# Optimization experiments

Hardware: AMD Instinct MI355X
Metric: run time of the kernel (lower is better)

## Reference

```python
import math
import jax, jax.numpy as jnp
import numpy as np

B, CIN, H, W = 1, 64, 56, 56
MID, HEADS, COUT, MPOS = 32, 8, 64, 56


def setup_inputs() -> dict:
    key = jax.random.key(0)
    ks = jax.random.split(key, 11)
    s = 0.05
    return {
        "x": jax.random.normal(ks[0], (B, CIN, H, W), jnp.float32),
        "Wq": jax.random.normal(ks[1], (MID * HEADS, CIN), jnp.float32) * s,
        "bq": jax.random.normal(ks[2], (MID * HEADS,), jnp.float32) * s,
        "Wk": jax.random.normal(ks[3], (MID * HEADS, CIN), jnp.float32) * s,
        "bk": jax.random.normal(ks[4], (MID * HEADS,), jnp.float32) * s,
        "Wv": jax.random.normal(ks[5], (MID * HEADS, CIN), jnp.float32) * s,
        "bv": jax.random.normal(ks[6], (MID * HEADS,), jnp.float32) * s,
        "Wo": jax.random.normal(ks[7], (COUT, MID * HEADS), jnp.float32) * s,
        "bo": jax.random.normal(ks[8], (COUT,), jnp.float32) * s,
        "row_emb_table": jax.random.normal(ks[9], (2 * MPOS - 1, MID // 2), jnp.float32) * s,
        "col_emb_table": jax.random.normal(ks[10], (2 * MPOS - 1, MID // 2), jnp.float32) * s,
    }


def _conv1x1(x, Wt, bt):
    # 1x1 Conv2d == channel-wise linear
    return jnp.einsum('bcij,dc->bdij', x, Wt) + bt[None, :, None, None]


def reference(x, Wq, bq, Wk, bk, Wv, bv, Wo, bo, row_emb_table, col_emb_table):
    b, cin, h, w = x.shape
    inv = 1.0 / math.sqrt(cin)
    q = _conv1x1(x, Wq, bq).reshape(b, MID, HEADS, h, w)
    k = _conv1x1(x, Wk, bk).reshape(b, MID, HEADS, h, w)
    # relative position indices (constant, derived from arange)
    rel = (jnp.arange(MPOS)[None, :] - jnp.arange(MPOS)[:, None]) + MPOS - 1
    row_emb = row_emb_table[rel[:w, :w].reshape(-1)].T.reshape(MID // 2, w, w)
    col_emb = col_emb_table[rel[:h, :h].reshape(-1)].T.reshape(MID // 2, h, h)
    q_row, q_col = q[:, :MID // 2], q[:, MID // 2:]
    row_scores = jnp.einsum('bchij,cik->bhijk', q_row, row_emb)  # [b,H,h,w,h]
    col_scores = jnp.einsum('bchij,cjl->bhijl', q_col, col_emb)  # [b,H,h,w,w]
    scores = (row_scores[..., :, None] + col_scores[..., None, :]) * inv
    scores = scores + jnp.einsum('bchij,bchkl->bhijkl', q, k) * inv  # [b,H,h,w,h,w]
    probs = jax.nn.softmax(scores.reshape(b, HEADS, h, w, -1), axis=-1).reshape(scores.shape)
    v = _conv1x1(x, Wv, bv).reshape(b, MID, HEADS, h, w)
    o = jnp.einsum('bhijkl,bchkl->bchij', probs, v)
    out = _conv1x1(o.reshape(b, MID * HEADS, h, w), Wo, bo)
    return out
```

## Files before the change

kernel.cpp:

```cpp
#include <hip/hip_runtime.h>

#define HW    3136
#define CIN   64
#define MIDC  32
#define HEADS 8
#define DTOT  256
#define COUTC 64
#define WDIM  56
#define QT    32
#define L2E   1.4426950408889634f

typedef unsigned int uint_t;
typedef _Float16 f16;
typedef __attribute__((ext_vector_type(8))) _Float16 half8;
typedef __attribute__((ext_vector_type(2))) __fp16  fp16x2;
typedef __attribute__((ext_vector_type(4))) float f32x4;

union HU { fp16x2 h; uint_t u; };
__device__ __forceinline__ uint_t pkh(float a, float b) {
    HU u; u.h = __builtin_amdgcn_cvt_pkrtz(a, b); return u.u;
}

__global__ __launch_bounds__(256) void qkv_fused_kernel(
    const float* __restrict__ x,
    const float* __restrict__ Wq, const float* __restrict__ bq,
    const float* __restrict__ Wk, const float* __restrict__ bk,
    const float* __restrict__ Wv, const float* __restrict__ bv,
    f16* __restrict__ qh, f16* __restrict__ kh, f16* __restrict__ vh)
{
    __shared__ float xs[64][36];
    __shared__ float Wlq[64][34];
    __shared__ float Wlk[64][34];
    __shared__ float Wlv[64][34];

    const int tid = threadIdx.x;
    const int h   = blockIdx.y;
    const int P0  = blockIdx.x * 32;

    {   int c = tid >> 2, g = tid & 3;
        const float* src = &x[(size_t)c * HW + P0 + g * 8];
        float4 v0 = *(const float4*)src;
        float4 v1 = *(const float4*)(src + 4);
        *(float4*)&xs[c][g * 8]     = v0;
        *(float4*)&xs[c][g * 8 + 4] = v1;
    }
    {   int m = tid >> 3, c8 = (tid & 7) * 8;
        size_t row = (size_t)(m * HEADS + h) * CIN + c8;
        float4 a0 = *(const float4*)&Wq[row], a1 = *(const float4*)&Wq[row + 4];
        float4 b0 = *(const float4*)&Wk[row], b1 = *(const float4*)&Wk[row + 4];
        float4 c0 = *(const float4*)&Wv[row], c1 = *(const float4*)&Wv[row + 4];
        #pragma unroll
        for (int i = 0; i < 4; ++i) {
            Wlq[c8 + i][m]     = ((const float*)&a0)[i];
            Wlq[c8 + 4 + i][m] = ((const float*)&a1)[i];
            Wlk[c8 + i][m]     = ((const float*)&b0)[i];
            Wlk[c8 + 4 + i][m] = ((const float*)&b1)[i];
            Wlv[c8 + i][m]     = ((const float*)&c0)[i];
            Wlv[c8 + 4 + i][m] = ((const float*)&c1)[i];
        }
    }
    __syncthreads();

    const int a  = tid & 15, pg = tid >> 4;
    const int m0 = a * 2,    p0 = pg * 2;
    const int d0 = m0 * HEADS + h, d1 = d0 + HEADS;

    float q00 = bq[d0], q01 = q00, q10 = bq[d1], q11 = q10;
    float k00 = bk[d0], k01 = k00, k10 = bk[d1], k11 = k10;
    float v00 = bv[d0], v01 = v00, v10 = bv[d1], v11 = v10;

    #pragma unroll 8
    for (int c = 0; c < CIN; ++c) {
        float x0 = xs[c][p0], x1 = xs[c][p0 + 1];
        float wq0 = Wlq[c][m0], wq1 = Wlq[c][m0 + 1];
        float wk0 = Wlk[c][m0], wk1 = Wlk[c][m0 + 1];
        float wv0 = Wlv[c][m0], wv1 = Wlv[c][m0 + 1];
        q00 += wq0 * x0; q01 += wq0 * x1; q10 += wq1 * x0; q11 += wq1 * x1;
        k00 += wk0 * x0; k01 += wk0 * x1; k10 += wk1 * x0; k11 += wk1 * x1;
        v00 += wv0 * x0; v01 += wv0 * x1; v10 += wv1 * x0; v11 += wv1 * x1;
    }

    size_t qk0 = (size_t)h * HW * MIDC + (size_t)(P0 + p0) * MIDC + m0;
    *(uint_t*)&qh[qk0]        = pkh(q00, q10);
    *(uint_t*)&qh[qk0 + MIDC] = pkh(q01, q11);
    *(uint_t*)&kh[qk0]        = pkh(k00, k10);
    *(uint_t*)&kh[qk0 + MIDC] = pkh(k01, k11);
    size_t vb0 = (size_t)(h * MIDC + m0) * HW + P0 + p0;
    *(uint_t*)&vh[vb0]      = pkh(v00, v01);
    *(uint_t*)&vh[vb0 + HW] = pkh(v10, v11);
}

__global__ __launch_bounds__(256, 3) void attn_kernel(
    const f16* __restrict__ qh, const f16* __restrict__ kh,
    const f16* __restrict__ vh,
    const float* __restrict__ rowt, const float* __restrict__ colt,
    float* __restrict__ ob)
{
    __shared__ f16   Qs[QT][MIDC];
    __shared__ float Rb[QT][57];
    __shared__ float Cb[QT][60];
    __shared__ __align__(16) char pool[18944];
    f16* PlBase = (f16*)pool;

    const int tid   = threadIdx.x;
    const int wave  = tid >> 6, lane = tid & 63;
    const int h     = blockIdx.y;
    const int qbase = blockIdx.x * QT;
    const float c1  = 0.125f * L2E;

    const f16* Qh = qh + (size_t)h * HW * MIDC;
    const f16* Kh = kh + (size_t)h * HW * MIDC;
    const f16* Vh = vh + (size_t)h * MIDC * HW;

    if (tid < 128) {
        int r = tid >> 2, c = (tid & 3) * 8;
        *(uint4*)&Qs[r][c] = *(const uint4*)&Qh[(size_t)(qbase + r) * MIDC + c];
    }
    __syncthreads();

    {
        int q = tid >> 3, sub = tid & 7;
        int qg = qbase + q, qi = qg / WDIM, qj = qg % WDIM;
        half8 qr0 = *(const half8*)&Qs[q][0];
        half8 qr1 = *(const half8*)&Qs[q][8];
        half8 qr2 = *(const half8*)&Qs[q][16];
        half8 qr3 = *(const half8*)&Qs[q][24];
        for (int kp = sub; kp < WDIM; kp += 8) {
            const float* rt = &rowt[(kp - qi + WDIM - 1) * 16];
            const float* ct = &colt[(kp - qj + WDIM - 1) * 16];
            float s = 0.f, s2 = 0.f;
            #pragma unroll
            for (int c = 0; c < 8; ++c) {
                s  += (float)qr0[c] * rt[c] + (float)qr1[c] * rt[8 + c];
                s2 += (float)qr2[c] * ct[c] + (float)qr3[c] * ct[8 + c];
            }
            Rb[q][kp] = s * c1;
            Cb[q][kp] = s2 * c1;
        }
    }
    __syncthreads();

    const int qL  = lane & 15;
    const int grp = lane >> 4;
    half8 qfrag[2];
    qfrag[0] = *(const half8*)&Qs[qL][grp * 8];
    qfrag[1] = *(const half8*)&Qs[16 + qL][grp * 8];

    float lacc[2] = {0.f, 0.f};
    f32x4 o[2][2];
    #pragma unroll
    for (int i = 0; i < 2; ++i) { o[i][0] = (f32x4){0,0,0,0}; o[i][1] = (f32x4){0,0,0,0}; }

    int ki_s[8], kj_s[8];
    #pragma unroll
    for (int s = 0; s < 8; ++s) {
        int key0 = wave * 128 + s * 16 + grp * 4;
        ki_s[s] = key0 / WDIM;
        kj_s[s] = key0 % WDIM;
    }

    f16* Pw = PlBase + wave * (16 * 136);

    for (int j = 0; j < 6; ++j) {
        const int base = 512 * j + 128 * wave;

        half8 kfr[8];
        #pragma unroll
        for (int s = 0; s < 8; ++s)
            kfr[s] = *(const half8*)&Kh[(size_t)(base + s*16 + qL) * MIDC + grp*8];
        half8 vfr[2][4];
        #pragma unroll
        for (int ch = 0; ch < 2; ++ch)
            #pragma unroll
            for (int kf2 = 0; kf2 < 4; ++kf2)
                vfr[ch][kf2] = *(const half8*)
                    &Vh[(size_t)(ch*16 + qL) * HW + base + kf2*32 + grp*8];

        #pragma unroll
        for (int hf = 0; hf < 2; ++hf) {
            const int qrow = hf * 16 + qL;
            f32x4 sc[8];
            #pragma unroll
            for (int s = 0; s < 8; ++s) {
                f32x4 z = {0.f,0.f,0.f,0.f};
                sc[s] = __builtin_amdgcn_mfma_f32_16x16x32_f16(kfr[s], qfrag[hf], z, 0,0,0);
            }
            #pragma unroll
            for (int s = 0; s < 8; ++s) {
                float rb = Rb[qrow][ki_s[s]];
                float4 cbv = *(const float4*)&Cb[qrow][kj_s[s]];
                float e0 = __builtin_amdgcn_exp2f(fmaf(sc[s][0], c1, rb + cbv.x));
                float e1 = __builtin_amdgcn_exp2f(fmaf(sc[s][1], c1, rb + cbv.y));
                float e2 = __builtin_amdgcn_exp2f(fmaf(sc[s][2], c1, rb + cbv.z));
                float e3 = __builtin_amdgcn_exp2f(fmaf(sc[s][3], c1, rb + cbv.w));
                lacc[hf] += (e0 + e1) + (e2 + e3);
                uint2 w2; w2.x = pkh(e0, e1); w2.y = pkh(e2, e3);
                *(uint2*)&Pw[qL * 136 + s * 16 + grp * 4] = w2;
            }
            #pragma unroll
            for (int kf2 = 0; kf2 < 4; ++kf2) {
                half8 pf = *(const half8*)&Pw[qL * 136 + kf2 * 32 + grp * 8];
                o[hf][0] = __builtin_amdgcn_mfma_f32_16x16x32_f16(vfr[0][kf2], pf, o[hf][0], 0,0,0);
                o[hf][1] = __builtin_amdgcn_mfma_f32_16x16x32_f16(vfr[1][kf2], pf, o[hf][1], 0,0,0);
            }
        }

        #pragma unroll
        for (int s = 0; s < 8; ++s) {
            kj_s[s] += 8;
            if (kj_s[s] >= WDIM) { kj_s[s] -= WDIM; ki_s[s] += 10; }
            else                 { ki_s[s] += 9; }
        }
    }

    if (wave == 0) {
        const int base = 3072;
        half8 kfr[4];
        #pragma unroll
        for (int s = 0; s < 4; ++s)
            kfr[s] = *(const half8*)&Kh[(size_t)(base + s*16 + qL) * MIDC + grp*8];
        half8 vfr[2][2];
        #pragma unroll
        for (int ch = 0; ch < 2; ++ch)
            #pragma unroll
            for (int kf2 = 0; kf2 < 2; ++kf2)
                vfr[ch][kf2] = *(const half8*)
                    &Vh[(size_t)(ch*16 + qL) * HW + base + kf2*32 + grp*8];
        #pragma unroll
        for (int hf = 0; hf < 2; ++hf) {
            const int qrow = hf * 16 + qL;
            f32x4 sc[4];
            #pragma unroll
            for (int s = 0; s < 4; ++s) {
                f32x4 z = {0.f,0.f,0.f,0.f};
                sc[s] = __builtin_amdgcn_mfma_f32_16x16x32_f16(kfr[s], qfrag[hf], z, 0,0,0);
            }
            #pragma unroll
            for (int s = 0; s < 4; ++s) {
                int key0 = base + s * 16 + grp * 4;
                int ki = key0 / WDIM, kj = key0 % WDIM;
                float rb = Rb[qrow][ki];
                float4 cbv = *(const float4*)&Cb[qrow][kj];
                float e0 = __builtin_amdgcn_exp2f(fmaf(sc[s][0], c1, rb + cbv.x));
                float e1 = __builtin_amdgcn_exp2f(fmaf(sc[s][1], c1, rb + cbv.y));
                float e2 = __builtin_amdgcn_exp2f(fmaf(sc[s][2], c1, rb + cbv.z));
                float e3 = __builtin_amdgcn_exp2f(fmaf(sc[s][3], c1, rb + cbv.w));
                lacc[hf] += (e0 + e1) + (e2 + e3);
                uint2 w2; w2.x = pkh(e0, e1); w2.y = pkh(e2, e3);
                *(uint2*)&Pw[qL * 136 + s * 16 + grp * 4] = w2;
            }
            #pragma unroll
            for (int kf2 = 0; kf2 < 2; ++kf2) {
                half8 pf = *(const half8*)&Pw[qL * 136 + kf2 * 32 + grp * 8];
                o[hf][0] = __builtin_amdgcn_mfma_f32_16x16x32_f16(vfr[0][kf2], pf, o[hf][0], 0,0,0);
                o[hf][1] = __builtin_amdgcn_mfma_f32_16x16x32_f16(vfr[1][kf2], pf, o[hf][1], 0,0,0);
            }
        }
    }

    #pragma unroll
    for (int hf = 0; hf < 2; ++hf) {
        lacc[hf] += __shfl_xor(lacc[hf], 16);
        lacc[hf] += __shfl_xor(lacc[hf], 32);
    }

    __syncthreads();
    float* MOb = (float*)pool;
    float* Ll  = MOb + 4 * 32 * 36;
    #pragma unroll
    for (int hf = 0; hf < 2; ++hf) {
        int row = wave * 32 + hf * 16 + qL;
        *(f32x4*)&MOb[row * 36 + grp * 4]      = o[hf][0];
        *(f32x4*)&MOb[row * 36 + 16 + grp * 4] = o[hf][1];
        if (grp == 0) Ll[row] = lacc[hf];
    }
    __syncthreads();

    {
        int q = tid & 31, cseg = tid >> 5;
        float l = (Ll[q] + Ll[32+q]) + (Ll[64+q] + Ll[96+q]);
        float invl = 1.f / l;
        int qg = qbase + q;
        #pragma unroll
        for (int i = 0; i < 4; ++i) {
            int ch = cseg * 4 + i;
            float acc = 0.f;
            #pragma unroll
            for (int w = 0; w < 4; ++w)
                acc += MOb[(w*32 + q) * 36 + ch];
            ob[(size_t)(ch * HEADS + h) * HW + qg] = acc * invl;
        }
    }
}

__global__ __launch_bounds__(64) void outproj_kernel(
    const float* __restrict__ ob, const float* __restrict__ Wo,
    const float* __restrict__ bo, float* __restrict__ out)
{
    const int lane = threadIdx.x;
    const int qL = lane & 15, grp = lane >> 4;
    const int p = blockIdx.x * 16 + qL;

    f32x4 acc[4];
    #pragma unroll
    for (int mt = 0; mt < 4; ++mt) acc[mt] = (f32x4){0,0,0,0};

    #pragma unroll
    for (int ks = 0; ks < 8; ++ks) {
        half8 bf;
        #pragma unroll
        for (int jj = 0; jj < 8; ++jj)
            bf[jj] = (f16)ob[(size_t)(ks * 32 + grp * 8 + jj) * HW + p];
        #pragma unroll
        for (int mt = 0; mt < 4; ++mt) {
            const float* wrow = &Wo[(size_t)(mt * 16 + qL) * DTOT + ks * 32 + grp * 8];
            float4 a0 = *(const float4*)wrow;
            float4 a1 = *(const float4*)(wrow + 4);
            half8 af;
            af[0] = (f16)a0.x; af[1] = (f16)a0.y; af[2] = (f16)a0.z; af[3] = (f16)a0.w;
            af[4] = (f16)a1.x; af[5] = (f16)a1.y; af[6] = (f16)a1.z; af[7] = (f16)a1.w;
            acc[mt] = __builtin_amdgcn_mfma_f32_16x16x32_f16(af, bf, acc[mt], 0, 0, 0);
        }
    }

    #pragma unroll
    for (int mt = 0; mt < 4; ++mt)
        #pragma unroll
        for (int r = 0; r < 4; ++r) {
            int d = mt * 16 + grp * 4 + r;
            out[(size_t)d * HW + p] = acc[mt][r] + bo[d];
        }
}

extern "C" void kernel_launch(void* const* d_in, const int* in_sizes, int n_in,
                              void* d_out, int out_size, void* d_ws, size_t ws_size,
                              hipStream_t stream)
{
    const float* x    = (const float*)d_in[0];
    const float* Wq   = (const float*)d_in[1];
    const float* bq   = (const float*)d_in[2];
    const float* Wk   = (const float*)d_in[3];
    const float* bk   = (const float*)d_in[4];
    const float* Wv   = (const float*)d_in[5];
    const float* bv   = (const float*)d_in[6];
    const float* Wo   = (const float*)d_in[7];
    const float* bo   = (const float*)d_in[8];
    const float* rowt = (const float*)d_in[9];
    const float* colt = (const float*)d_in[10];
    float* out = (float*)d_out;

    const size_t N = (size_t)DTOT * HW;
    f16* qh = (f16*)d_ws;
    f16* kh = qh + N;
    f16* vh = kh + N;
    float* ob = (float*)(vh + N);

    qkv_fused_kernel<<<dim3(HW / 32, HEADS), 256, 0, stream>>>(
        x, Wq, bq, Wk, bk, Wv, bv, qh, kh, vh);
    attn_kernel<<<dim3(HW / QT, HEADS), 256, 0, stream>>>(qh, kh, vh, rowt, colt, ob);
    outproj_kernel<<<dim3(HW / 16), 64, 0, stream>>>(ob, Wo, bo, out);
}
```

Measured before the change: 146.2 us.

## Split attention key range across two blocks and merge partial sums in outproj

Adds a grid z-dimension that splits the key range of each query tile into two halves. Each half writes unnormalized partial outputs and partial softmax denominators to separate buffers. The output projection kernel then adds the two partials and normalizes before the MFMA. Launch bounds are also raised to 4 blocks per CU. The goal is more blocks in flight and better CU utilization on a grid that was small. The cost is duplicated per-block Q and position-embedding setup, extra workspace, and doubled partial-output traffic into outproj.

```diff
diff --git a/kernel.cpp b/kernel.cpp
--- a/kernel.cpp
+++ b/kernel.cpp
@@ -90,11 +90,12 @@
     *(uint_t*)&vh[vb0 + HW] = pkh(v10, v11);
 }
 
-__global__ __launch_bounds__(256, 3) void attn_kernel(
+__global__ __launch_bounds__(256, 4) void attn_kernel(
     const f16* __restrict__ qh, const f16* __restrict__ kh,
     const f16* __restrict__ vh,
     const float* __restrict__ rowt, const float* __restrict__ colt,
-    float* __restrict__ ob)
+    float* __restrict__ ob0, float* __restrict__ ob1,
+    float* __restrict__ lb)
 {
     __shared__ f16   Qs[QT][MIDC];
     __shared__ float Rb[QT][57];
@@ -105,8 +106,11 @@
     const int tid   = threadIdx.x;
     const int wave  = tid >> 6, lane = tid & 63;
     const int h     = blockIdx.y;
+    const int half  = blockIdx.z;
     const int qbase = blockIdx.x * QT;
     const float c1  = 0.125f * L2E;
+
+    float* __restrict__ obp = half ? ob1 : ob0;
 
     const f16* Qh = qh + (size_t)h * HW * MIDC;
     const f16* Kh = kh + (size_t)h * HW * MIDC;
@@ -154,15 +158,15 @@
     int ki_s[8], kj_s[8];
     #pragma unroll
     for (int s = 0; s < 8; ++s) {
-        int key0 = wave * 128 + s * 16 + grp * 4;
+        int key0 = half * 1536 + wave * 128 + s * 16 + grp * 4;
         ki_s[s] = key0 / WDIM;
         kj_s[s] = key0 % WDIM;
     }
 
     f16* Pw = PlBase + wave * (16 * 136);
 
-    for (int j = 0; j < 6; ++j) {
-        const int base = 512 * j + 128 * wave;
+    for (int j = 0; j < 3; ++j) {
+        const int base = half * 1536 + 512 * j + 128 * wave;
 
         half8 kfr[8];
         #pragma unroll
@@ -213,7 +217,7 @@
         }
     }
 
-    if (wave == 0) {
+    if (half == 1 && wave == 0) {
         const int base = 3072;
         half8 kfr[4];
         #pragma unroll
@@ -278,8 +282,6 @@
 
     {
         int q = tid & 31, cseg = tid >> 5;
-        float l = (Ll[q] + Ll[32+q]) + (Ll[64+q] + Ll[96+q]);
-        float invl = 1.f / l;
         int qg = qbase + q;
         #pragma unroll
         for (int i = 0; i < 4; ++i) {
@@ -288,19 +290,30 @@
             #pragma unroll
             for (int w = 0; w < 4; ++w)
                 acc += MOb[(w*32 + q) * 36 + ch];
-            ob[(size_t)(ch * HEADS + h) * HW + qg] = acc * invl;
+            obp[(size_t)(ch * HEADS + h) * HW + qg] = acc;
+        }
+        if (cseg == 0) {
+            float l = (Ll[q] + Ll[32+q]) + (Ll[64+q] + Ll[96+q]);
+            lb[(size_t)(half * HEADS + h) * HW + qg] = l;
         }
     }
 }
 
 __global__ __launch_bounds__(64) void outproj_kernel(
-    const float* __restrict__ ob, const float* __restrict__ Wo,
-    const float* __restrict__ bo, float* __restrict__ out)
+    const float* __restrict__ ob0, const float* __restrict__ ob1,
+    const float* __restrict__ lb,
+    const float* __restrict__ Wo, const float* __restrict__ bo,
+    float* __restrict__ out)
 {
     const int lane = threadIdx.x;
     const int qL = lane & 15, grp = lane >> 4;
     const int p = blockIdx.x * 16 + qL;
 
+    float invl[8];
+    #pragma unroll
+    for (int hh = 0; hh < 8; ++hh)
+        invl[hh] = 1.f / (lb[(size_t)hh * HW + p] + lb[(size_t)(8 + hh) * HW + p]);
+
     f32x4 acc[4];
     #pragma unroll
     for (int mt = 0; mt < 4; ++mt) acc[mt] = (f32x4){0,0,0,0};
@@ -309,8 +322,10 @@
     for (int ks = 0; ks < 8; ++ks) {
         half8 bf;
         #pragma unroll
-        for (int jj = 0; jj < 8; ++jj)
-            bf[jj] = (f16)ob[(size_t)(ks * 32 + grp * 8 + jj) * HW + p];
+        for (int jj = 0; jj < 8; ++jj) {
+            size_t idx = (size_t)(ks * 32 + grp * 8 + jj) * HW + p;
+            bf[jj] = (f16)((ob0[idx] + ob1[idx]) * invl[jj]);
+        }
         #pragma unroll
         for (int mt = 0; mt < 4; ++mt) {
             const float* wrow = &Wo[(size_t)(mt * 16 + qL) * DTOT + ks * 32 + grp * 8];
@@ -353,10 +368,13 @@
     f16* qh = (f16*)d_ws;
     f16* kh = qh + N;
     f16* vh = kh + N;
-    float* ob = (float*)(vh + N);
+    float* ob0 = (float*)(vh + N);
+    float* ob1 = ob0 + N;
+    float* lb  = ob1 + N;
 
     qkv_fused_kernel<<<dim3(HW / 32, HEADS), 256, 0, stream>>>(
         x, Wq, bq, Wk, bk, Wv, bv, qh, kh, vh);
-    attn_kernel<<<dim3(HW / QT, HEADS), 256, 0, stream>>>(qh, kh, vh, rowt, colt, ob);
-    outproj_kernel<<<dim3(HW / 16), 64, 0, stream>>>(ob, Wo, bo, out);
-}
+    attn_kernel<<<dim3(HW / QT, HEADS, 2), 256, 0, stream>>>(
+        qh, kh, vh, rowt, colt, ob0, ob1, lb);
+    outproj_kernel<<<dim3(HW / 16), 64, 0, stream>>>(ob0, ob1, lb, Wo, bo, out);
+}
```

New measurement: 210.6 us. +44.1%, slower.

## Store attention output as position-major fp16 and stage permuted Wo in LDS

Applied to the files above, without the earlier changes.

The attention kernel now writes its normalized output as fp16 in a position-major [HW][256] layout, using head-major channel order, with packed 8-byte stores. Previously it wrote fp32 channel-major with strided scalar stores. The output projection reads each half8 operand with one contiguous load. It converts Wo once per block into a column-permuted fp16 LDS tile matching the new channel order, and runs 4 waves per block. This cuts intermediate traffic and the strided gathers, at the cost of per-block Wo staging and an extra fp16 rounding step on the attention output.

```diff
diff --git a/kernel.cpp b/kernel.cpp
--- a/kernel.cpp
+++ b/kernel.cpp
@@ -94,7 +94,7 @@
     const f16* __restrict__ qh, const f16* __restrict__ kh,
     const f16* __restrict__ vh,
     const float* __restrict__ rowt, const float* __restrict__ colt,
-    float* __restrict__ ob)
+    f16* __restrict__ obf)
 {
     __shared__ f16   Qs[QT][MIDC];
     __shared__ float Rb[QT][57];
@@ -281,25 +281,45 @@
         float l = (Ll[q] + Ll[32+q]) + (Ll[64+q] + Ll[96+q]);
         float invl = 1.f / l;
         int qg = qbase + q;
-        #pragma unroll
-        for (int i = 0; i < 4; ++i) {
-            int ch = cseg * 4 + i;
-            float acc = 0.f;
-            #pragma unroll
-            for (int w = 0; w < 4; ++w)
-                acc += MOb[(w*32 + q) * 36 + ch];
-            ob[(size_t)(ch * HEADS + h) * HW + qg] = acc * invl;
-        }
-    }
-}
-
-__global__ __launch_bounds__(64) void outproj_kernel(
-    const float* __restrict__ ob, const float* __restrict__ Wo,
+        float a0 = 0.f, a1 = 0.f, a2 = 0.f, a3 = 0.f;
+        #pragma unroll
+        for (int w = 0; w < 4; ++w) {
+            const float* r = &MOb[(w*32 + q) * 36 + cseg * 4];
+            a0 += r[0]; a1 += r[1]; a2 += r[2]; a3 += r[3];
+        }
+        uint2 pk;
+        pk.x = pkh(a0 * invl, a1 * invl);
+        pk.y = pkh(a2 * invl, a3 * invl);
+        *(uint2*)&obf[(size_t)qg * DTOT + h * MIDC + cseg * 4] = pk;
+    }
+}
+
+__global__ __launch_bounds__(256) void outproj_kernel(
+    const f16* __restrict__ obf, const float* __restrict__ Wo,
     const float* __restrict__ bo, float* __restrict__ out)
 {
-    const int lane = threadIdx.x;
+    __shared__ f16  WoL[64][264];
+    __shared__ float bol[64];
+
+    const int tid = threadIdx.x;
+    {
+        int d = tid >> 2, part = tid & 3;
+        const float* wr = &Wo[(size_t)d * DTOT];
+        #pragma unroll
+        for (int i = 0; i < 32; ++i) {
+            int cc = part * 64 + i * 2;
+            int h0 = cc >> 5, m0 = cc & 31;
+            float w0 = wr[m0 * 8 + h0];
+            float w1 = wr[(m0 + 1) * 8 + h0];
+            *(uint_t*)&WoL[d][cc] = pkh(w0, w1);
+        }
+        if (tid < 64) bol[tid] = bo[tid];
+    }
+    __syncthreads();
+
+    const int wave = tid >> 6, lane = tid & 63;
     const int qL = lane & 15, grp = lane >> 4;
-    const int p = blockIdx.x * 16 + qL;
+    const int p = blockIdx.x * 64 + wave * 16 + qL;
 
     f32x4 acc[4];
     #pragma unroll
@@ -307,18 +327,10 @@
 
     #pragma unroll
     for (int ks = 0; ks < 8; ++ks) {
-        half8 bf;
-        #pragma unroll
-        for (int jj = 0; jj < 8; ++jj)
-            bf[jj] = (f16)ob[(size_t)(ks * 32 + grp * 8 + jj) * HW + p];
+        half8 bf = *(const half8*)&obf[(size_t)p * DTOT + ks * 32 + grp * 8];
         #pragma unroll
         for (int mt = 0; mt < 4; ++mt) {
-            const float* wrow = &Wo[(size_t)(mt * 16 + qL) * DTOT + ks * 32 + grp * 8];
-            float4 a0 = *(const float4*)wrow;
-            float4 a1 = *(const float4*)(wrow + 4);
-            half8 af;
-            af[0] = (f16)a0.x; af[1] = (f16)a0.y; af[2] = (f16)a0.z; af[3] = (f16)a0.w;
-            af[4] = (f16)a1.x; af[5] = (f16)a1.y; af[6] = (f16)a1.z; af[7] = (f16)a1.w;
+            half8 af = *(const half8*)&WoL[mt * 16 + qL][ks * 32 + grp * 8];
             acc[mt] = __builtin_amdgcn_mfma_f32_16x16x32_f16(af, bf, acc[mt], 0, 0, 0);
         }
     }
@@ -328,7 +340,7 @@
         #pragma unroll
         for (int r = 0; r < 4; ++r) {
             int d = mt * 16 + grp * 4 + r;
-            out[(size_t)d * HW + p] = acc[mt][r] + bo[d];
+            out[(size_t)d * HW + p] = acc[mt][r] + bol[d];
         }
 }
 
@@ -350,13 +362,14 @@
     float* out = (float*)d_out;
 
     const size_t N = (size_t)DTOT * HW;
-    f16* qh = (f16*)d_ws;
-    f16* kh = qh + N;
-    f16* vh = kh + N;
-    float* ob = (float*)(vh + N);
+    f16* qh  = (f16*)d_ws;
+    f16* kh  = qh + N;
+    f16* vh  = kh + N;
+    f16* obf = vh + N;
 
     qkv_fused_kernel<<<dim3(HW / 32, HEADS), 256, 0, stream>>>(
         x, Wq, bq, Wk, bk, Wv, bv, qh, kh, vh);
-    attn_kernel<<<dim3(HW / QT, HEADS), 256, 0, stream>>>(qh, kh, vh, rowt, colt, ob);
-    outproj_kernel<<<dim3(HW / 16), 64, 0, stream>>>(ob, Wo, bo, out);
-}
+    attn_kernel<<<dim3(HW / QT, HEADS), 256, 0, stream>>>(
+        qh, kh, vh, rowt, colt, obf);
+    outproj_kernel<<<dim3(HW / 64), 256, 0, stream>>>(obf, Wo, bo, out);
+}
```

After: 149.9 us (median of 2 runs). 2.5% more time.
